# Kernel optimization log

Measured on AMD Instinct MI355X. Metric: run time of the kernel, lower is better.

Reference implementation:

```python
import jax, jax.numpy as jnp
import numpy as np

B, LP, LQ, H = 16, 1024, 1024, 1024


def setup_inputs() -> dict:
    key = jax.random.key(0)
    k1, k2, k3 = jax.random.split(key, 3)
    p = jax.random.normal(k1, (B, LP, H), dtype=jnp.float32)
    q = jax.random.normal(k2, (B, LQ, H), dtype=jnp.float32)
    # Dense(hidden_size) kernel + bias (glorot-ish scale)
    W_key = jax.random.normal(k3, (H, H), dtype=jnp.float32) / np.sqrt(H)
    b_key = jnp.zeros((H,), dtype=jnp.float32)
    return {"p": p, "q": q, "W_key": W_key, "b_key": b_key}


def reference(p, q, W_key, b_key):
    # keys = Dense(q): [B, LQ, H]
    keys = jnp.einsum("bqh,hk->bqk", q, W_key) + b_key
    # attention scores p @ keys^T (no scaling): [B, LP, LQ]
    scores = jnp.einsum("bph,bqh->bpq", p, keys)
    attn = jax.nn.softmax(scores, axis=-1)
    # q reused as values; relu on output: [B, LP, H]
    out = jax.nn.relu(jnp.einsum("bpq,bqh->bph", attn, q))
    return out
```

## Files before the change

### kernel.cpp

```cpp
#include <hip/hip_runtime.h>
#include <hip/hip_bf16.h>

#define B_N 16
#define LP_N 1024
#define LQ_N 1024
#define H_N 1024

typedef unsigned short u16;
typedef __attribute__((ext_vector_type(8))) _Float16 f16x8;
typedef __attribute__((ext_vector_type(4))) float f32x4;

__device__ __forceinline__ u16 f2h(float x) {
    _Float16 h = (_Float16)x;
    return *(u16*)&h;
}
__device__ __forceinline__ float h2f(u16 u) {
    _Float16 h;
    *(u16*)&h = u;
    return (float)h;
}

__device__ __forceinline__ void load_lds16(const u16* g, u16* l) {
    __builtin_amdgcn_global_load_lds(
        (const __attribute__((address_space(1))) void*)g,
        (__attribute__((address_space(3))) void*)l, 16, 0, 0);
}

#define MFMA_F16(a, b, c) __builtin_amdgcn_mfma_f32_16x16x32_f16(a, b, c, 0, 0, 0)
#define VMW0()  asm volatile("s_waitcnt vmcnt(0)" ::: "memory")
#define VMW4()  asm volatile("s_waitcnt vmcnt(4)" ::: "memory")
#define LGKM8() asm volatile("s_waitcnt lgkmcnt(8)" ::: "memory")
#define LGKM0() asm volatile("s_waitcnt lgkmcnt(0)" ::: "memory")
#define SCHB()  __builtin_amdgcn_sched_barrier(0)
#define SBAR()  __builtin_amdgcn_s_barrier()

template<bool SPLIT, int EPI>
__launch_bounds__(512, 2)
__global__ void gemm2t(const u16* __restrict__ Ahi, const u16* __restrict__ Alo,
                       const u16* __restrict__ Bm,
                       const float* __restrict__ bias,
                       float* __restrict__ Cf, u16* __restrict__ Ch,
                       int N, int gn, int gmn,
                       long long sA, long long sB, long long sC)
{
    constexpr int REG  = 8192;
    constexpr int O_AL = REG;
    constexpr int O_B  = SPLIT ? 2 * REG : REG;
    constexpr int BUF  = SPLIT ? 3 * REG : 2 * REG;
    __shared__ __align__(16) u16 lds[2 * BUF];

    const int tid  = threadIdx.x;
    const int lane = tid & 63;
    const int wv   = tid >> 6;
    const int wr   = wv >> 2, wc = wv & 3;

    const int d   = blockIdx.x;
    const int cpx = gridDim.x >> 3;
    const int swz = (d & 7) * cpx + (d >> 3);
    const long long z = swz / gmn;
    const int r_  = swz % gmn;
    const int bm  = (r_ / gn) * 256;
    const int bn  = (r_ % gn) * 256;

    const char* pAh = (const char*)(Ahi + z * sA);
    const char* pAl = (const char*)(Alo + z * sA);
    const char* pB  = (const char*)(Bm + z * sB);

    const int r0 = tid >> 2;
    const int xc = (tid & 3) ^ ((r0 >> 1) & 3);
    const long long aof = (long long)(bm + r0) * 2048 + xc * 16;
    const long long bof = (long long)(bn + r0) * 2048 + xc * 16;
    const long long ao2 = aof + 128 * 2048;
    const long long bo2 = bof + 128 * 2048;
    const int d0 = tid * 8;
    const int d1 = d0 + 4096;

    int offA[8], offB[4];
#pragma unroll
    for (int i = 0; i < 8; ++i) {
        const int r = wr * 128 + i * 16 + (lane & 15);
        offA[i] = r * 32 + ((((lane >> 4) ^ (r >> 1)) & 3) << 3);
    }
#pragma unroll
    for (int j = 0; j < 4; ++j) {
        const int r = wc * 64 + j * 16 + (lane & 15);
        offB[j] = r * 32 + ((((lane >> 4) ^ (r >> 1)) & 3) << 3);
    }

    f32x4 acc[8][4];
#pragma unroll
    for (int i = 0; i < 8; ++i)
#pragma unroll
        for (int j = 0; j < 4; ++j)
            acc[i][j] = (f32x4){0.f, 0.f, 0.f, 0.f};

#define STG(NB, KB) do {                                                      \
        load_lds16((const u16*)(pAh + aof + (KB)), lds + (NB) + d0);          \
        load_lds16((const u16*)(pAh + ao2 + (KB)), lds + (NB) + d1);          \
        load_lds16((const u16*)(pB + bof + (KB)), lds + (NB) + O_B + d0);     \
        load_lds16((const u16*)(pB + bo2 + (KB)), lds + (NB) + O_B + d1);     \
        if constexpr (SPLIT) {                                                \
            load_lds16((const u16*)(pAl + aof + (KB)), lds + (NB) + O_AL + d0); \
            load_lds16((const u16*)(pAl + ao2 + (KB)), lds + (NB) + O_AL + d1); \
        }                                                                     \
    } while (0)

#define TERM(AF, BF) do {                                                     \
        __builtin_amdgcn_s_setprio(1);                                        \
        _Pragma("unroll")                                                     \
        for (int i = 0; i < 8; ++i)                                           \
            _Pragma("unroll")                                                 \
            for (int j = 0; j < 4; ++j)                                       \
                acc[i][j] = MFMA_F16(AF[i], BF[j], acc[i][j]);                \
        __builtin_amdgcn_s_setprio(0);                                        \
    } while (0)

    constexpr int NT = 32;

    STG(0, 0);

    for (int t = 0; t < NT; ++t) {
        const int cb = (t & 1) ? BUF : 0;
        const int nb = (t & 1) ? 0 : BUF;
        const long long kb = (long long)(t + 1) * 64;

        VMW0();
        SBAR();
        f16x8 b[4], ah[8], al[8];
#pragma unroll
        for (int j = 0; j < 4; ++j)
            b[j] = *(const f16x8*)(lds + cb + O_B + offB[j]);
#pragma unroll
        for (int i = 0; i < 8; ++i)
            ah[i] = *(const f16x8*)(lds + cb + offA[i]);
        if constexpr (SPLIT) {
#pragma unroll
            for (int i = 0; i < 8; ++i)
                al[i] = *(const f16x8*)(lds + cb + O_AL + offA[i]);
        }
        if (t + 1 < NT) STG(nb, kb);
        if constexpr (SPLIT) { LGKM8(); } else { LGKM0(); }
        SCHB();
        TERM(ah, b);
        if constexpr (SPLIT) {
            LGKM0(); SCHB();
            TERM(al, b);
        }
    }
#undef STG
#undef TERM

    const long long Cbase = z * sC;
#pragma unroll
    for (int i = 0; i < 8; ++i) {
        const int row0 = bm + wr * 128 + i * 16 + ((lane >> 4) << 2);
#pragma unroll
        for (int j = 0; j < 4; ++j) {
            const int col = bn + wc * 64 + j * 16 + (lane & 15);
#pragma unroll
            for (int e = 0; e < 4; ++e) {
                const float v = acc[i][j][e];
                const long long idx = Cbase + (long long)(row0 + e) * N + col;
                if constexpr (EPI == 0) {
                    Cf[idx] = v;
                } else if constexpr (EPI == 1) {
                    Ch[idx] = f2h(v + bias[col]);
                } else {
                    Cf[idx] = fmaxf(v, 0.f);
                }
            }
        }
    }
}

template<int EPI>
__launch_bounds__(512, 2)
__global__ void gemm_d2(const u16* __restrict__ Am, const u16* __restrict__ Bm,
                        float* __restrict__ Cf,
                        int N, int gn, int gmn,
                        long long sA, long long sB, long long sC)
{
    constexpr int REG = 8192;
    constexpr int O_B = REG;
    constexpr int BUF = 2 * REG;
    __shared__ __align__(16) u16 lds[3 * BUF];

    const int tid  = threadIdx.x;
    const int lane = tid & 63;
    const int wv   = tid >> 6;
    const int wr   = wv >> 2, wc = wv & 3;

    const int d   = blockIdx.x;
    const int cpx = gridDim.x >> 3;
    const int swz = (d & 7) * cpx + (d >> 3);
    const long long z = swz / gmn;
    const int r_  = swz % gmn;
    const int bm  = (r_ / gn) * 256;
    const int bn  = (r_ % gn) * 256;

    const char* pA = (const char*)(Am + z * sA);
    const char* pB = (const char*)(Bm + z * sB);

    const int r0 = tid >> 2;
    const int xc = (tid & 3) ^ ((r0 >> 1) & 3);
    const long long aof = (long long)(bm + r0) * 2048 + xc * 16;
    const long long bof = (long long)(bn + r0) * 2048 + xc * 16;
    const long long ao2 = aof + 128 * 2048;
    const long long bo2 = bof + 128 * 2048;
    const int d0 = tid * 8;
    const int d1 = d0 + 4096;

    int offA[8], offB[4];
#pragma unroll
    for (int i = 0; i < 8; ++i) {
        const int r = wr * 128 + i * 16 + (lane & 15);
        offA[i] = r * 32 + ((((lane >> 4) ^ (r >> 1)) & 3) << 3);
    }
#pragma unroll
    for (int j = 0; j < 4; ++j) {
        const int r = wc * 64 + j * 16 + (lane & 15);
        offB[j] = r * 32 + ((((lane >> 4) ^ (r >> 1)) & 3) << 3);
    }

    f32x4 acc[8][4];
#pragma unroll
    for (int i = 0; i < 8; ++i)
#pragma unroll
        for (int j = 0; j < 4; ++j)
            acc[i][j] = (f32x4){0.f, 0.f, 0.f, 0.f};

#define STG(NB, KB) do {                                                      \
        load_lds16((const u16*)(pA + aof + (KB)), lds + (NB) + d0);           \
        load_lds16((const u16*)(pA + ao2 + (KB)), lds + (NB) + d1);           \
        load_lds16((const u16*)(pB + bof + (KB)), lds + (NB) + O_B + d0);     \
        load_lds16((const u16*)(pB + bo2 + (KB)), lds + (NB) + O_B + d1);     \
    } while (0)

#define TERM(AF, BF) do {                                                     \
        __builtin_amdgcn_s_setprio(1);                                        \
        _Pragma("unroll")                                                     \
        for (int i = 0; i < 8; ++i)                                           \
            _Pragma("unroll")                                                 \
            for (int j = 0; j < 4; ++j)                                       \
                acc[i][j] = MFMA_F16(AF[i], BF[j], acc[i][j]);                \
        __builtin_amdgcn_s_setprio(0);                                        \
    } while (0)

    constexpr int NT = 32;

    STG(0, 0);
    STG(BUF, 64);

    int cb = 0;
    for (int t = 0; t < NT; ++t) {
        if (t + 1 < NT) { VMW4(); } else { VMW0(); }
        SBAR();
        f16x8 b[4], a[8];
#pragma unroll
        for (int j = 0; j < 4; ++j)
            b[j] = *(const f16x8*)(lds + cb + O_B + offB[j]);
#pragma unroll
        for (int i = 0; i < 8; ++i)
            a[i] = *(const f16x8*)(lds + cb + offA[i]);
        if (t + 2 < NT) {
            const int nb = (cb + 2 * BUF) % (3 * BUF);
            STG(nb, (long long)(t + 2) * 64);
        }
        LGKM0(); SCHB();
        TERM(a, b);
        cb += BUF;
        if (cb == 3 * BUF) cb = 0;
    }
#undef STG
#undef TERM

    const long long Cbase = z * sC;
#pragma unroll
    for (int i = 0; i < 8; ++i) {
        const int row0 = bm + wr * 128 + i * 16 + ((lane >> 4) << 2);
#pragma unroll
        for (int j = 0; j < 4; ++j) {
            const int col = bn + wc * 64 + j * 16 + (lane & 15);
#pragma unroll
            for (int e = 0; e < 4; ++e) {
                const float v = acc[i][j][e];
                const long long idx = Cbase + (long long)(row0 + e) * N + col;
                if constexpr (EPI == 0) Cf[idx] = v;
                else                    Cf[idx] = fmaxf(v, 0.f);
            }
        }
    }
}

__global__ void cvt_f16(const float* __restrict__ in, u16* __restrict__ o16,
                        long long n4)
{
    const long long i = (long long)blockIdx.x * 256 + threadIdx.x;
    if (i >= n4) return;
    const float4 v = ((const float4*)in)[i];
    ushort4 h;
    h.x = f2h(v.x); h.y = f2h(v.y); h.z = f2h(v.z); h.w = f2h(v.w);
    ((ushort4*)o16)[i] = h;
}

__global__ void fuse_cvt_q(const float* __restrict__ q, u16* __restrict__ hi,
                           u16* __restrict__ lo, u16* __restrict__ thi)
{
    __shared__ float t[32][33];
    const long long z = blockIdx.z;
    const long long base = z * 1048576;
    const int r0 = blockIdx.y * 32, c0 = blockIdx.x * 32;
    for (int j = threadIdx.y; j < 32; j += 8) {
        const float v = q[base + (long long)(r0 + j) * 1024 + c0 + threadIdx.x];
        t[j][threadIdx.x] = v;
        const long long o = base + (long long)(r0 + j) * 1024 + c0 + threadIdx.x;
        const u16 h = f2h(v);
        hi[o] = h;
        lo[o] = f2h(v - h2f(h));
    }
    __syncthreads();
    for (int j = threadIdx.y; j < 32; j += 8)
        thi[base + (long long)(c0 + j) * 1024 + r0 + threadIdx.x] = f2h(t[threadIdx.x][j]);
}

__global__ void transpose_cvt_w(const float* __restrict__ in, u16* __restrict__ hi)
{
    __shared__ float t[32][33];
    const int r0 = blockIdx.y * 32, c0 = blockIdx.x * 32;
    for (int j = threadIdx.y; j < 32; j += 8)
        t[j][threadIdx.x] = in[(long long)(r0 + j) * 1024 + c0 + threadIdx.x];
    __syncthreads();
    for (int j = threadIdx.y; j < 32; j += 8)
        hi[(long long)(c0 + j) * 1024 + r0 + threadIdx.x] = f2h(t[threadIdx.x][j]);
}

__global__ void softmax_f16(const float* __restrict__ S, u16* __restrict__ A)
{
    const long long row = blockIdx.x;
    const float* r = S + row * (long long)LQ_N;
    const int t = threadIdx.x;
    float4 v = ((const float4*)r)[t];

    float m = fmaxf(fmaxf(v.x, v.y), fmaxf(v.z, v.w));
#pragma unroll
    for (int off = 32; off > 0; off >>= 1)
        m = fmaxf(m, __shfl_xor(m, off));

    __shared__ float red[4];
    const int lane = t & 63, wid = t >> 6;
    if (lane == 0) red[wid] = m;
    __syncthreads();
    m = fmaxf(fmaxf(red[0], red[1]), fmaxf(red[2], red[3]));
    __syncthreads();

    v.x = __expf(v.x - m); v.y = __expf(v.y - m);
    v.z = __expf(v.z - m); v.w = __expf(v.w - m);
    float s = v.x + v.y + v.z + v.w;
#pragma unroll
    for (int off = 32; off > 0; off >>= 1)
        s += __shfl_xor(s, off);
    if (lane == 0) red[wid] = s;
    __syncthreads();
    s = red[0] + red[1] + red[2] + red[3];

    const float inv = 1.0f / s;
    ushort4 o;
    o.x = f2h(v.x * inv); o.y = f2h(v.y * inv);
    o.z = f2h(v.z * inv); o.w = f2h(v.w * inv);
    ((ushort4*)(A + row * (long long)LQ_N))[t] = o;
}

#define BM 128
#define BN 128
#define BK 8
#define TM 8
#define TN 8

template<bool TRANSB, bool BIAS, bool RELU>
__launch_bounds__(256)
__global__ void gemm_k(const float* __restrict__ A, const float* __restrict__ Bmat,
                       const float* __restrict__ bias, float* __restrict__ C,
                       int M, int N, int K,
                       long long sA, long long sB, long long sC)
{
    __shared__ float As[BK][BM];
    __shared__ float Bs[BK][BN];
    const int tid = threadIdx.x;
    const int tx = tid & 15;
    const int ty = tid >> 4;
    const int bn = blockIdx.x * BN;
    const int bm = blockIdx.y * BM;
    const long long z = blockIdx.z;
    A += z * sA; Bmat += z * sB; C += z * sC;
    float acc[TM][TN];
#pragma unroll
    for (int i = 0; i < TM; i++)
#pragma unroll
        for (int j = 0; j < TN; j++) acc[i][j] = 0.f;
    const int arow = tid >> 1;
    const int acol = (tid & 1) * 4;
    const int bk_n = tid >> 5;
    const int bn_n = (tid & 31) * 4;
    for (int k0 = 0; k0 < K; k0 += BK) {
        float4 a4 = *(const float4*)&A[(long long)(bm + arow) * K + k0 + acol];
        As[acol + 0][arow] = a4.x; As[acol + 1][arow] = a4.y;
        As[acol + 2][arow] = a4.z; As[acol + 3][arow] = a4.w;
        if (TRANSB) {
            float4 b4 = *(const float4*)&Bmat[(long long)(bn + arow) * K + k0 + acol];
            Bs[acol + 0][arow] = b4.x; Bs[acol + 1][arow] = b4.y;
            Bs[acol + 2][arow] = b4.z; Bs[acol + 3][arow] = b4.w;
        } else {
            float4 b4 = *(const float4*)&Bmat[(long long)(k0 + bk_n) * N + bn + bn_n];
            *(float4*)&Bs[bk_n][bn_n] = b4;
        }
        __syncthreads();
#pragma unroll
        for (int k = 0; k < BK; k++) {
            float a[TM], b[TN];
            *(float4*)&a[0] = *(const float4*)&As[k][ty * TM];
            *(float4*)&a[4] = *(const float4*)&As[k][ty * TM + 4];
            *(float4*)&b[0] = *(const float4*)&Bs[k][tx * TN];
            *(float4*)&b[4] = *(const float4*)&Bs[k][tx * TN + 4];
#pragma unroll
            for (int i = 0; i < TM; i++)
#pragma unroll
                for (int j = 0; j < TN; j++)
                    acc[i][j] = fmaf(a[i], b[j], acc[i][j]);
        }
        __syncthreads();
    }
#pragma unroll
    for (int i = 0; i < TM; i++) {
        const int row = bm + ty * TM + i;
#pragma unroll
        for (int j = 0; j < TN; j += 4) {
            const int col = bn + tx * TN + j;
            float4 v;
            v.x = acc[i][j + 0]; v.y = acc[i][j + 1];
            v.z = acc[i][j + 2]; v.w = acc[i][j + 3];
            if (BIAS) {
                v.x += bias[col + 0]; v.y += bias[col + 1];
                v.z += bias[col + 2]; v.w += bias[col + 3];
            }
            if (RELU) {
                v.x = fmaxf(v.x, 0.f); v.y = fmaxf(v.y, 0.f);
                v.z = fmaxf(v.z, 0.f); v.w = fmaxf(v.w, 0.f);
            }
            *(float4*)&C[(long long)row * N + col] = v;
        }
    }
}

__global__ void softmax_k(float* __restrict__ S)
{
    const long long row = blockIdx.x;
    float* r = S + row * (long long)LQ_N;
    const int t = threadIdx.x;
    float4 v = ((float4*)r)[t];
    float m = fmaxf(fmaxf(v.x, v.y), fmaxf(v.z, v.w));
#pragma unroll
    for (int off = 32; off > 0; off >>= 1)
        m = fmaxf(m, __shfl_xor(m, off));
    __shared__ float red[4];
    const int lane = t & 63, wid = t >> 6;
    if (lane == 0) red[wid] = m;
    __syncthreads();
    m = fmaxf(fmaxf(red[0], red[1]), fmaxf(red[2], red[3]));
    __syncthreads();
    v.x = __expf(v.x - m); v.y = __expf(v.y - m);
    v.z = __expf(v.z - m); v.w = __expf(v.w - m);
    float s = v.x + v.y + v.z + v.w;
#pragma unroll
    for (int off = 32; off > 0; off >>= 1)
        s += __shfl_xor(s, off);
    if (lane == 0) red[wid] = s;
    __syncthreads();
    s = red[0] + red[1] + red[2] + red[3];
    const float inv = 1.0f / s;
    v.x *= inv; v.y *= inv; v.z *= inv; v.w *= inv;
    ((float4*)r)[t] = v;
}

extern "C" void kernel_launch(void* const* d_in, const int* in_sizes, int n_in,
                              void* d_out, int out_size, void* d_ws, size_t ws_size,
                              hipStream_t stream)
{
    const float* p    = (const float*)d_in[0];
    const float* q    = (const float*)d_in[1];
    const float* W    = (const float*)d_in[2];
    const float* bias = (const float*)d_in[3];
    float* out = (float*)d_out;

    const size_t MB32 = 33554432ull;
    const size_t NEED = 5 * MB32 + 2097152ull;

    if (ws_size >= NEED) {
        char* w = (char*)d_ws;
        u16* p16   = (u16*)(w + 0 * MB32);
        u16* q_hi  = (u16*)(w + 1 * MB32);
        u16* q_lo  = (u16*)(w + 2 * MB32);
        u16* keys  = (u16*)(w + 3 * MB32);
        u16* qT    = (u16*)(w + 4 * MB32);
        u16* Wt    = (u16*)(w + 5 * MB32);
        float* scores = (float*)(w + 1 * MB32);
        u16* attn     = (u16*)(w + 0 * MB32);

        const long long n4 = (long long)B_N * LQ_N * H_N / 4;
        cvt_f16<<<dim3((unsigned)(n4 / 256)), 256, 0, stream>>>(p, p16, n4);
        fuse_cvt_q<<<dim3(32, 32, B_N), dim3(32, 8), 0, stream>>>(q, q_hi, q_lo, qT);
        transpose_cvt_w<<<dim3(32, 32, 1), dim3(32, 8), 0, stream>>>(W, Wt);

        gemm2t<true, 1><<<256, 512, 0, stream>>>(
            q_hi, q_lo, Wt, bias, nullptr, keys,
            H_N, 4, 256, 0, 0, 0);

        gemm_d2<0><<<256, 512, 0, stream>>>(
            p16, keys, scores,
            LQ_N, 4, 16,
            (long long)LP_N * H_N, (long long)LQ_N * H_N, (long long)LP_N * LQ_N);

        softmax_f16<<<B_N * LP_N, 256, 0, stream>>>(scores, attn);

        gemm_d2<2><<<256, 512, 0, stream>>>(
            attn, qT, out,
            H_N, 4, 16,
            (long long)LP_N * LQ_N, (long long)H_N * LQ_N, (long long)LP_N * H_N);
    } else {
        float* keys   = (float*)d_ws;
        float* scores = keys + (long long)B_N * LQ_N * H_N;

        gemm_k<false, true, false><<<dim3(H_N / BN, (B_N * LQ_N) / BM, 1), 256, 0, stream>>>(
            q, W, bias, keys, B_N * LQ_N, H_N, H_N, 0, 0, 0);
        gemm_k<true, false, false><<<dim3(LQ_N / BN, LP_N / BM, B_N), 256, 0, stream>>>(
            p, keys, nullptr, scores, LP_N, LQ_N, H_N,
            (long long)LP_N * H_N, (long long)LQ_N * H_N, (long long)LP_N * LQ_N);
        softmax_k<<<B_N * LP_N, 256, 0, stream>>>(scores);
        gemm_k<false, false, true><<<dim3(H_N / BN, LP_N / BM, B_N), 256, 0, stream>>>(
            scores, q, nullptr, out, LP_N, H_N, LQ_N,
            (long long)LP_N * LQ_N, (long long)LQ_N * H_N, (long long)LP_N * H_N);
    }
}
```

Baseline: 229.6 us.

## Restructure batched GEMM into 8-phase ping-pong pipeline with K=128 tiles

Replaces the triple-buffered K=64 main loop of the batched f16 GEMM with a double-buffered K=128 loop split into eight phases per two tiles. Each phase reads two A fragments, issues a slice of the next global-to-LDS loads, and runs a block of MFMAs, so loads are spread across the compute instead of issued in bursts. The LDS swizzle widens to 8 chunks per 128-wide row. The aim is better overlap of memory traffic and MFMA and fewer loop iterations, at the cost of more barriers per tile and a 128 KB LDS footprint, which may limit occupancy compared with the previous 96 KB.

Result: faster. 221.4 us (-3.6%).

```diff
diff --git a/kernel.cpp b/kernel.cpp
--- a/kernel.cpp
+++ b/kernel.cpp
@@ -175,15 +175,14 @@
 
 template<int EPI>
 __launch_bounds__(512, 2)
-__global__ void gemm_d2(const u16* __restrict__ Am, const u16* __restrict__ Bm,
+__global__ void gemm_p8(const u16* __restrict__ Am, const u16* __restrict__ Bm,
                         float* __restrict__ Cf,
                         int N, int gn, int gmn,
                         long long sA, long long sB, long long sC)
 {
-    constexpr int REG = 8192;
-    constexpr int O_B = REG;
-    constexpr int BUF = 2 * REG;
-    __shared__ __align__(16) u16 lds[3 * BUF];
+    constexpr int OB    = 16384;
+    constexpr int BUFSZ = 32768;
+    __shared__ __align__(16) u16 lds[2 * BUFSZ];
 
     const int tid  = threadIdx.x;
     const int lane = tid & 63;
@@ -201,25 +200,29 @@
     const char* pA = (const char*)(Am + z * sA);
     const char* pB = (const char*)(Bm + z * sB);
 
-    const int r0 = tid >> 2;
-    const int xc = (tid & 3) ^ ((r0 >> 1) & 3);
-    const long long aof = (long long)(bm + r0) * 2048 + xc * 16;
-    const long long bof = (long long)(bn + r0) * 2048 + xc * 16;
-    const long long ao2 = aof + 128 * 2048;
-    const long long bo2 = bof + 128 * 2048;
-    const int d0 = tid * 8;
-    const int d1 = d0 + 4096;
-
-    int offA[8], offB[4];
+    const int rr  = tid >> 3;
+    const int xcv = (tid & 7) ^ (rr & 7);
+    long long aofs[4], bofs[4];
+#pragma unroll
+    for (int j = 0; j < 4; ++j) {
+        aofs[j] = (long long)(bm + rr + j * 64) * 2048 + xcv * 16;
+        bofs[j] = (long long)(bn + rr + j * 64) * 2048 + xcv * 16;
+    }
+
+    int offA[8][2], offB[4][2];
 #pragma unroll
     for (int i = 0; i < 8; ++i) {
         const int r = wr * 128 + i * 16 + (lane & 15);
-        offA[i] = r * 32 + ((((lane >> 4) ^ (r >> 1)) & 3) << 3);
+#pragma unroll
+        for (int s = 0; s < 2; ++s)
+            offA[i][s] = r * 64 + ((((s * 4 + (lane >> 4)) ^ r) & 7) << 3);
     }
 #pragma unroll
     for (int j = 0; j < 4; ++j) {
         const int r = wc * 64 + j * 16 + (lane & 15);
-        offB[j] = r * 32 + ((((lane >> 4) ^ (r >> 1)) & 3) << 3);
+#pragma unroll
+        for (int s = 0; s < 2; ++s)
+            offB[j][s] = OB + r * 64 + ((((s * 4 + (lane >> 4)) ^ r) & 7) << 3);
     }
 
     f32x4 acc[8][4];
@@ -229,50 +232,71 @@
         for (int j = 0; j < 4; ++j)
             acc[i][j] = (f32x4){0.f, 0.f, 0.f, 0.f};
 
-#define STG(NB, KB) do {                                                      \
-        load_lds16((const u16*)(pA + aof + (KB)), lds + (NB) + d0);           \
-        load_lds16((const u16*)(pA + ao2 + (KB)), lds + (NB) + d1);           \
-        load_lds16((const u16*)(pB + bof + (KB)), lds + (NB) + O_B + d0);     \
-        load_lds16((const u16*)(pB + bo2 + (KB)), lds + (NB) + O_B + d1);     \
+    f16x8 bb[4][2];
+
+#define STA(NB, J, KB) load_lds16((const u16*)(pA + aofs[J] + (KB)), \
+                                  lds + (NB) + tid * 8 + (J) * 4096)
+#define STB(NB, J, KB) load_lds16((const u16*)(pB + bofs[J] + (KB)), \
+                                  lds + (NB) + OB + tid * 8 + (J) * 4096)
+#define RD_BB(CB) do {                                                        \
+        _Pragma("unroll")                                                     \
+        for (int j = 0; j < 4; ++j) {                                         \
+            bb[j][0] = *(const f16x8*)(lds + (CB) + offB[j][0]);              \
+            bb[j][1] = *(const f16x8*)(lds + (CB) + offB[j][1]);              \
+        }                                                                     \
     } while (0)
-
-#define TERM(AF, BF) do {                                                     \
+#define PHASE(CB, I0, FIRST, STAGES, WAITST) do {                             \
+        if (FIRST) RD_BB(CB);                                                 \
+        f16x8 a00 = *(const f16x8*)(lds + (CB) + offA[(I0)][0]);              \
+        f16x8 a01 = *(const f16x8*)(lds + (CB) + offA[(I0)][1]);              \
+        f16x8 a10 = *(const f16x8*)(lds + (CB) + offA[(I0) + 1][0]);          \
+        f16x8 a11 = *(const f16x8*)(lds + (CB) + offA[(I0) + 1][1]);          \
+        STAGES;                                                               \
+        if (FIRST) LGKM8();                                                   \
+        SBAR();                                                               \
+        LGKM0(); SCHB();                                                      \
         __builtin_amdgcn_s_setprio(1);                                        \
         _Pragma("unroll")                                                     \
-        for (int i = 0; i < 8; ++i)                                           \
-            _Pragma("unroll")                                                 \
-            for (int j = 0; j < 4; ++j)                                       \
-                acc[i][j] = MFMA_F16(AF[i], BF[j], acc[i][j]);                \
+        for (int j = 0; j < 4; ++j) {                                         \
+            acc[(I0)][j]     = MFMA_F16(a00, bb[j][0], acc[(I0)][j]);         \
+            acc[(I0)][j]     = MFMA_F16(a01, bb[j][1], acc[(I0)][j]);         \
+            acc[(I0) + 1][j] = MFMA_F16(a10, bb[j][0], acc[(I0) + 1][j]);     \
+            acc[(I0) + 1][j] = MFMA_F16(a11, bb[j][1], acc[(I0) + 1][j]);     \
+        }                                                                     \
         __builtin_amdgcn_s_setprio(0);                                        \
+        WAITST;                                                               \
+        SBAR();                                                               \
     } while (0)
 
-    constexpr int NT = 32;
-
-    STG(0, 0);
-    STG(BUF, 64);
-
-    int cb = 0;
-    for (int t = 0; t < NT; ++t) {
-        if (t + 1 < NT) { VMW4(); } else { VMW0(); }
-        SBAR();
-        f16x8 b[4], a[8];
-#pragma unroll
-        for (int j = 0; j < 4; ++j)
-            b[j] = *(const f16x8*)(lds + cb + O_B + offB[j]);
-#pragma unroll
-        for (int i = 0; i < 8; ++i)
-            a[i] = *(const f16x8*)(lds + cb + offA[i]);
-        if (t + 2 < NT) {
-            const int nb = (cb + 2 * BUF) % (3 * BUF);
-            STG(nb, (long long)(t + 2) * 64);
-        }
-        LGKM0(); SCHB();
-        TERM(a, b);
-        cb += BUF;
-        if (cb == 3 * BUF) cb = 0;
-    }
-#undef STG
-#undef TERM
+    constexpr int NT2 = 8;
+
+    STB(0, 0, 0); STB(0, 1, 0); STB(0, 2, 0); STB(0, 3, 0);
+    STA(0, 0, 0); STA(0, 1, 0); STA(0, 2, 0); STA(0, 3, 0);
+    STB(BUFSZ, 0, 128); STB(BUFSZ, 1, 128); STB(BUFSZ, 2, 128); STB(BUFSZ, 3, 128);
+    VMW4();
+    SBAR();
+
+    for (int it = 0; it < NT2; ++it) {
+        const long long kb1 = (long long)(2 * it + 1) * 128;
+        const long long kb2 = (long long)(2 * it + 2) * 128;
+        const long long kb3 = (long long)(2 * it + 3) * 128;
+        const bool st2 = (it + 1) < NT2;
+
+        PHASE(0, 0, true,  { STA(BUFSZ, 0, kb1); STA(BUFSZ, 1, kb1); }, );
+        PHASE(0, 2, false, { STA(BUFSZ, 2, kb1); STA(BUFSZ, 3, kb1); }, );
+        PHASE(0, 4, false, { if (st2) { STB(0, 0, kb2); STB(0, 1, kb2); } }, );
+        PHASE(0, 6, false, { if (st2) { STB(0, 2, kb2); STB(0, 3, kb2); } },
+              { if (st2) { VMW4(); } else { VMW0(); } });
+        PHASE(BUFSZ, 0, true,  { if (st2) { STA(0, 0, kb2); STA(0, 1, kb2); } }, );
+        PHASE(BUFSZ, 2, false, { if (st2) { STA(0, 2, kb2); STA(0, 3, kb2); } }, );
+        PHASE(BUFSZ, 4, false, { if (st2) { STB(BUFSZ, 0, kb3); STB(BUFSZ, 1, kb3); } }, );
+        PHASE(BUFSZ, 6, false, { if (st2) { STB(BUFSZ, 2, kb3); STB(BUFSZ, 3, kb3); } },
+              { if (st2) VMW4(); });
+    }
+#undef STA
+#undef STB
+#undef RD_BB
+#undef PHASE
 
     const long long Cbase = z * sC;
 #pragma unroll
@@ -514,14 +538,14 @@
             q_hi, q_lo, Wt, bias, nullptr, keys,
             H_N, 4, 256, 0, 0, 0);
 
-        gemm_d2<0><<<256, 512, 0, stream>>>(
+        gemm_p8<0><<<256, 512, 0, stream>>>(
             p16, keys, scores,
             LQ_N, 4, 16,
             (long long)LP_N * H_N, (long long)LQ_N * H_N, (long long)LP_N * LQ_N);
 
         softmax_f16<<<B_N * LP_N, 256, 0, stream>>>(scores, attn);
 
-        gemm_d2<2><<<256, 512, 0, stream>>>(
+        gemm_p8<2><<<256, 512, 0, stream>>>(
             attn, qT, out,
             H_N, 4, 16,
             (long long)LP_N * LQ_N, (long long)H_N * LQ_N, (long long)LP_N * H_N);
```
